# Kernel tuning notes

Hardware: AMD Instinct MI355X
Metric: run time of the kernel (lower is better)

The kernel has to match this reference:

```python
import jax, jax.numpy as jnp
import numpy as np

D_MODEL, D_FF, N_EXPERTS, TOP_K = 1024, 4096, 8, 2
LN_EPS = 1e-5


def setup_inputs() -> dict:
    key = jax.random.key(0)
    ks = jax.random.split(key, 9)
    s = 0.02
    return {
        "x": jax.random.normal(ks[0], (4, 2048, D_MODEL), dtype=jnp.float32),
        "Wg": jax.random.normal(ks[1], (D_MODEL, N_EXPERTS), dtype=jnp.float32) * s,
        "bg": jnp.zeros((N_EXPERTS,), dtype=jnp.float32),
        "W1": jax.random.normal(ks[2], (N_EXPERTS, D_MODEL, D_FF), dtype=jnp.float32) * s,
        "b1": jnp.zeros((N_EXPERTS, D_FF), dtype=jnp.float32),
        "W2": jax.random.normal(ks[3], (N_EXPERTS, D_FF, D_MODEL), dtype=jnp.float32) * s,
        "b2": jnp.zeros((N_EXPERTS, D_MODEL), dtype=jnp.float32),
        "gamma": jnp.ones((D_MODEL,), dtype=jnp.float32),
        "beta": jnp.zeros((D_MODEL,), dtype=jnp.float32),
    }


def _moe(x, Wg, bg, W1, b1, W2, b2, gamma, beta):
    B, S, D = x.shape
    xf = x.reshape(B * S, D)                       # (T, D)
    logits = xf @ Wg + bg                          # (T, E)
    probs = jax.nn.softmax(logits, axis=-1)
    topk_scores, topk_idx = jax.lax.top_k(probs, TOP_K)   # (T, K)
    # combine weights per expert: w[t, e] = sum_k score[t,k] * [idx[t,k]==e]
    onehot = jax.nn.one_hot(topk_idx, N_EXPERTS, dtype=probs.dtype)  # (T, K, E)
    w = jnp.einsum("tk,tke->te", topk_scores, onehot)                # (T, E)
    # load-balancing aux loss (switch-style): E * sum_e f_e * P_e
    f = jnp.mean(onehot, axis=(0, 1)) * 1.0        # fraction of routed slots per expert
    P = jnp.mean(probs, axis=0)
    aux_loss = jnp.float32(N_EXPERTS) * jnp.sum(f * P)
    # dense-equivalent expert compute; zero weight for unrouted tokens matches
    # the masked gather/scatter math of the original.
    out = jnp.zeros_like(xf)
    for e in range(N_EXPERTS):
        h = jax.nn.relu(xf @ W1[e] + b1[e])        # (T, D_FF)
        y = h @ W2[e] + b2[e]                      # (T, D)
        out = out + w[:, e:e + 1] * y
    out = out.reshape(B, S, D)
    # residual + post-layernorm (dropout disabled, eval mode)
    z = x + out
    mu = jnp.mean(z, axis=-1, keepdims=True)
    var = jnp.mean(jnp.square(z - mu), axis=-1, keepdims=True)
    z = (z - mu) * jax.lax.rsqrt(var + LN_EPS) * gamma + beta
    return z, aux_loss


def reference(x, Wg, bg, W1, b1, W2, b2, gamma, beta):
    return _moe(x, Wg, bg, W1, b1, W2, b2, gamma, beta)
```

## Files before the change

### kernel.cpp

```cpp
#include <hip/hip_runtime.h>

#define T_TOK 8192
#define DM    1024
#define DFF   4096
#define NE    8
#define CAP   2560
#define SLOTS (NE * CAP)
#define MTILES 20

typedef __attribute__((ext_vector_type(4))) float f32x4;
typedef __attribute__((ext_vector_type(8))) short bf16x8;
typedef __attribute__((ext_vector_type(4))) unsigned short u16x4;

__device__ __forceinline__ unsigned short f2bf(float f) {
  unsigned int u = __float_as_uint(f);
  u = (u + 0x7FFFu + ((u >> 16) & 1u)) >> 16;
  return (unsigned short)u;
}
__device__ __forceinline__ float bf2f(unsigned short u) {
  return __uint_as_float(((unsigned)u) << 16);
}

__device__ __forceinline__ void gld_lds16(const void* g, void* l) {
  __builtin_amdgcn_global_load_lds(
      (const __attribute__((address_space(1))) void*)g,
      (__attribute__((address_space(3))) void*)l, 16, 0, 0);
}

__device__ __forceinline__ bf16x8 ldsr(unsigned addr) {
  bf16x8 r;
  asm volatile("ds_read_b128 %0, %1" : "=v"(r) : "v"(addr));
  return r;
}

__global__ __launch_bounds__(256) void transpose_convert2(
    const float* __restrict__ W1, unsigned short* __restrict__ W1t,
    const float* __restrict__ W2, unsigned short* __restrict__ W2t)
{
  __shared__ float tile[64][65];
  int z = blockIdx.z;
  const float* W; unsigned short* Wt; int R, C, c0, r0;
  if (z < 8) {
    W = W1 + (size_t)z * DM * DFF; Wt = W1t + (size_t)z * DM * DFF;
    R = DM; C = DFF;
    c0 = blockIdx.x * 64; r0 = blockIdx.y * 64;
  } else {
    W = W2 + (size_t)(z - 8) * DM * DFF; Wt = W2t + (size_t)(z - 8) * DM * DFF;
    R = DFF; C = DM;
    c0 = (blockIdx.x & 15) * 64; r0 = (blockIdx.y * 4 + (blockIdx.x >> 4)) * 64;
  }
  int tid = threadIdx.x;
  int lr = tid >> 4, lc = (tid & 15) * 4;
#pragma unroll
  for (int i = 0; i < 4; ++i) {
    float4 v = *(const float4*)(W + (size_t)(r0 + i * 16 + lr) * C + c0 + lc);
    tile[i * 16 + lr][lc] = v.x; tile[i * 16 + lr][lc + 1] = v.y;
    tile[i * 16 + lr][lc + 2] = v.z; tile[i * 16 + lr][lc + 3] = v.w;
  }
  __syncthreads();
#pragma unroll
  for (int i = 0; i < 4; ++i) {
    int o = i * 256 + tid;
    int rq = o & 15, cw = o >> 4;
    u16x4 u;
    u.x = f2bf(tile[rq * 4 + 0][cw]); u.y = f2bf(tile[rq * 4 + 1][cw]);
    u.z = f2bf(tile[rq * 4 + 2][cw]); u.w = f2bf(tile[rq * 4 + 3][cw]);
    __builtin_nontemporal_store(u, (u16x4*)(Wt + (size_t)(c0 + cw) * R + r0 + rq * 4));
  }
}

__global__ __launch_bounds__(256) void router_kernel(
    const float* __restrict__ x, const float* __restrict__ Wg, const float* __restrict__ bg,
    int* __restrict__ slotOf, float* __restrict__ slot_w,
    int* __restrict__ pos, float* __restrict__ P_sh,
    unsigned short* __restrict__ Abuf)
{
  __shared__ float wgT[NE * DM];
  for (int i = threadIdx.x; i < NE * DM; i += 256) {
    int d = i >> 3, e = i & 7;
    wgT[e * DM + d] = Wg[i];
  }
  __syncthreads();
  int w = threadIdx.x >> 6, lane = threadIdx.x & 63;
  int sh = blockIdx.x & 63;
  for (int it = 0; it < 4; ++it) {
    int t = (blockIdx.x * 4 + w) * 4 + it;
    float4 xv[4];
    float p[NE];
#pragma unroll
    for (int e = 0; e < NE; ++e) p[e] = 0.f;
#pragma unroll
    for (int ps = 0; ps < 4; ++ps) {
      int d0 = ps * 256 + lane * 4;
      xv[ps] = *(const float4*)(x + (size_t)t * DM + d0);
#pragma unroll
      for (int e = 0; e < NE; ++e) {
        float4 wv = *(const float4*)(wgT + e * DM + d0);
        p[e] += xv[ps].x * wv.x + xv[ps].y * wv.y + xv[ps].z * wv.z + xv[ps].w * wv.w;
      }
    }
#pragma unroll
    for (int e = 0; e < NE; ++e) {
#pragma unroll
      for (int o = 1; o < 64; o <<= 1) p[e] += __shfl_xor(p[e], o);
      p[e] += bg[e];
    }
    float mx = p[0];
#pragma unroll
    for (int e = 1; e < NE; ++e) mx = fmaxf(mx, p[e]);
    float se = 0.f;
#pragma unroll
    for (int e = 0; e < NE; ++e) { p[e] = expf(p[e] - mx); se += p[e]; }
    float inv = 1.f / se;
#pragma unroll
    for (int e = 0; e < NE; ++e) p[e] *= inv;
    int e0 = 0; float v0 = p[0];
#pragma unroll
    for (int e = 1; e < NE; ++e) if (p[e] > v0) { v0 = p[e]; e0 = e; }
    int e1 = -1; float v1 = -1.f;
#pragma unroll
    for (int e = 0; e < NE; ++e) if (e != e0 && p[e] > v1) { v1 = p[e]; e1 = e; }
    int p0 = 0, p1 = 0;
    if (lane == 0) {
      p0 = atomicAdd(&pos[e0], 1);
      p1 = atomicAdd(&pos[e1], 1);
    }
    p0 = __shfl(p0, 0); p1 = __shfl(p1, 0);
    int s0 = e0 * CAP + (p0 < CAP ? p0 : CAP - 1);
    int s1 = e1 * CAP + (p1 < CAP ? p1 : CAP - 1);
    if (lane == 0) {
      slotOf[2 * t] = s0; slotOf[2 * t + 1] = s1;
      slot_w[s0] = v0; slot_w[s1] = v1;
#pragma unroll
      for (int e = 0; e < NE; ++e) atomicAdd(&P_sh[sh * 8 + e], p[e]);
    }
    unsigned short* d0p = Abuf + (size_t)s0 * DM;
    unsigned short* d1p = Abuf + (size_t)s1 * DM;
#pragma unroll
    for (int ps = 0; ps < 4; ++ps) {
      int d = ps * 256 + lane * 4;
      ushort4 u;
      u.x = f2bf(xv[ps].x); u.y = f2bf(xv[ps].y);
      u.z = f2bf(xv[ps].z); u.w = f2bf(xv[ps].w);
      *(ushort4*)(d0p + d) = u;
      *(ushort4*)(d1p + d) = u;
    }
  }
}

template<int KDIM, int EPI>
__global__ __launch_bounds__(256, 3) void moe_gemm(
    const unsigned short* __restrict__ A, const unsigned short* __restrict__ Bt,
    const float* __restrict__ bias, unsigned short* __restrict__ Out,
    const int* __restrict__ pos, const float* __restrict__ slot_w, int N)
{
  constexpr int KT = (EPI == 0 ? KDIM : KDIM / 2) / 32;
  int e, koff, sp;
  if (EPI == 0) { e = blockIdx.z; koff = 0; sp = 0; }
  else { e = blockIdx.z >> 1; sp = blockIdx.z & 1; koff = sp * (KDIM / 2); }

  int cnt = pos[e];
  if (cnt > CAP) cnt = CAP;

  int nx = N >> 7;
  int b = blockIdx.x + blockIdx.y * nx;
  int cpx = nx * MTILES / 8;
  int wg = (b & 7) * cpx + (b >> 3);
  int ntile = wg / MTILES, mt = wg % MTILES;
  if (mt * 128 >= cnt) return;
  int m0 = e * CAP + mt * 128, n0 = ntile * 128;

  __shared__ __align__(16) char lds[49152];

  const int tid = threadIdx.x, lane = tid & 63, w = tid >> 6;
  const int wr = w >> 1, wc = w & 1;

  const int ssl = 8 * ((tid & 3) ^ ((tid >> 3) & 3));
  const unsigned short* Asrc = A + (size_t)(m0 + (tid >> 2)) * KDIM + koff + ssl;
  const unsigned short* Bsrc = Bt + (size_t)e * N * KDIM + (size_t)(n0 + (tid >> 2)) * KDIM + koff + ssl;

  unsigned lbase = (unsigned)(size_t)(__attribute__((address_space(3))) char*)lds;
  const unsigned swz = 16u * (unsigned)((lane >> 4) ^ ((lane >> 1) & 3));
  const unsigned aoff = (unsigned)((wr * 64 + (lane & 15)) * 64) + swz;
  const unsigned boff = 8192u + (unsigned)((wc * 64 + (lane & 15)) * 64) + swz;

  f32x4 acc[4][4] = {};
  bf16x8 Aq[4], Bq[4];

#define STAGE(KT_, BUFO_)                                                    \
  { int k0_ = (KT_) * 32;                                                    \
    char* lb_ = lds + (BUFO_);                                               \
    gld_lds16(Asrc + k0_,                      lb_ + tid * 16);              \
    gld_lds16(Asrc + (size_t)64 * KDIM + k0_,  lb_ + 4096 + tid * 16);       \
    gld_lds16(Bsrc + k0_,                      lb_ + 8192 + tid * 16);       \
    gld_lds16(Bsrc + (size_t)64 * KDIM + k0_,  lb_ + 12288 + tid * 16); }

  STAGE(0, 0)
  STAGE(1, 16384)
  asm volatile("s_waitcnt vmcnt(4)" ::: "memory");
  __builtin_amdgcn_s_barrier();

  unsigned cur = 0;
#pragma unroll 1
  for (int kt = 0; kt < KT; ++kt) {
    unsigned bo = lbase + cur;
    if (kt + 2 < KT) {
      unsigned stg = cur + 32768u; if (stg >= 49152u) stg -= 49152u;
      STAGE(kt + 2, stg)
    }
#pragma unroll
    for (int mi = 0; mi < 4; ++mi) Aq[mi] = ldsr(bo + aoff + mi * 1024u);
#pragma unroll
    for (int ni = 0; ni < 4; ++ni) Bq[ni] = ldsr(bo + boff + ni * 1024u);
    asm volatile("s_waitcnt lgkmcnt(0)" ::: "memory");
    __builtin_amdgcn_sched_barrier(0);
    __builtin_amdgcn_s_setprio(1);
#pragma unroll
    for (int mi = 0; mi < 4; ++mi)
#pragma unroll
      for (int ni = 0; ni < 4; ++ni)
        acc[mi][ni] = __builtin_amdgcn_mfma_f32_16x16x32_bf16(
            Aq[mi], Bq[ni], acc[mi][ni], 0, 0, 0);
    __builtin_amdgcn_s_setprio(0);
    if (kt + 2 < KT)      asm volatile("s_waitcnt vmcnt(4)" ::: "memory");
    else if (kt + 1 < KT) asm volatile("s_waitcnt vmcnt(0)" ::: "memory");
    __builtin_amdgcn_s_barrier();
    cur += 16384u; if (cur == 49152u) cur = 0;
  }
#undef STAGE

  int cn = lane & 15;
  int r4 = (lane >> 4) * 4;
  if (EPI == 0) {
#pragma unroll
    for (int ni = 0; ni < 4; ++ni) {
      int col = n0 + wc * 64 + ni * 16 + cn;
      float bv = bias[e * N + col];
#pragma unroll
      for (int mi = 0; mi < 4; ++mi) {
        int row = m0 + wr * 64 + mi * 16 + r4;
#pragma unroll
        for (int j = 0; j < 4; ++j) {
          float v = acc[mi][ni][j] + bv;
          __builtin_nontemporal_store(f2bf(v > 0.f ? v : 0.f),
                                      Out + (size_t)(row + j) * N + col);
        }
      }
    }
  } else {
    unsigned short* Yw = Out + (size_t)sp * SLOTS * DM;
    float bv[4];
#pragma unroll
    for (int ni = 0; ni < 4; ++ni)
      bv[ni] = (sp == 0) ? bias[e * N + n0 + wc * 64 + ni * 16 + cn] : 0.f;
#pragma unroll
    for (int mi = 0; mi < 4; ++mi) {
      int rbase = m0 + wr * 64 + mi * 16 + r4;
#pragma unroll
      for (int j = 0; j < 4; ++j) {
        int slot = rbase + j;
        float wgt = slot_w[slot];
#pragma unroll
        for (int ni = 0; ni < 4; ++ni) {
          int col = n0 + wc * 64 + ni * 16 + cn;
          __builtin_nontemporal_store(f2bf(wgt * (acc[mi][ni][j] + bv[ni])),
                                      Yw + (size_t)slot * DM + col);
        }
      }
    }
  }
}

__global__ __launch_bounds__(256) void ln_kernel(
    const float* __restrict__ x, const unsigned short* __restrict__ Ybuf,
    const int* __restrict__ slotOf,
    const float* __restrict__ gamma, const float* __restrict__ beta,
    float* __restrict__ out)
{
  int t = blockIdx.x;
  int s0 = slotOf[2 * t], s1 = slotOf[2 * t + 1];
  const unsigned short* y00 = Ybuf + (size_t)s0 * DM;
  const unsigned short* y01 = Ybuf + (size_t)SLOTS * DM + (size_t)s0 * DM;
  const unsigned short* y10 = Ybuf + (size_t)s1 * DM;
  const unsigned short* y11 = Ybuf + (size_t)SLOTS * DM + (size_t)s1 * DM;
  int c = threadIdx.x * 4;
  float4 xv = *(const float4*)(x + (size_t)t * DM + c);
  ushort4 a0 = *(const ushort4*)(y00 + c);
  ushort4 a1 = *(const ushort4*)(y01 + c);
  ushort4 a2 = *(const ushort4*)(y10 + c);
  ushort4 a3 = *(const ushort4*)(y11 + c);
  float z[4];
  z[0] = xv.x + bf2f(a0.x) + bf2f(a1.x) + bf2f(a2.x) + bf2f(a3.x);
  z[1] = xv.y + bf2f(a0.y) + bf2f(a1.y) + bf2f(a2.y) + bf2f(a3.y);
  z[2] = xv.z + bf2f(a0.z) + bf2f(a1.z) + bf2f(a2.z) + bf2f(a3.z);
  z[3] = xv.w + bf2f(a0.w) + bf2f(a1.w) + bf2f(a2.w) + bf2f(a3.w);
  float s = z[0] + z[1] + z[2] + z[3];
  float s2 = z[0]*z[0] + z[1]*z[1] + z[2]*z[2] + z[3]*z[3];
#pragma unroll
  for (int o = 1; o < 64; o <<= 1) { s += __shfl_xor(s, o); s2 += __shfl_xor(s2, o); }
  __shared__ float ls[8];
  int w = threadIdx.x >> 6, lane = threadIdx.x & 63;
  if (lane == 0) { ls[w] = s; ls[4 + w] = s2; }
  __syncthreads();
  s = ls[0] + ls[1] + ls[2] + ls[3];
  s2 = ls[4] + ls[5] + ls[6] + ls[7];
  float mu = s * (1.f / DM);
  float var = s2 * (1.f / DM) - mu * mu;
  float rstd = rsqrtf(var + 1e-5f);
  float4 gv = *(const float4*)(gamma + c);
  float4 bv = *(const float4*)(beta + c);
  float4 ov;
  ov.x = (z[0] - mu) * rstd * gv.x + bv.x;
  ov.y = (z[1] - mu) * rstd * gv.y + bv.y;
  ov.z = (z[2] - mu) * rstd * gv.z + bv.z;
  ov.w = (z[3] - mu) * rstd * gv.w + bv.w;
  *(float4*)(out + (size_t)t * DM + c) = ov;
}

__global__ void aux_kernel(const float* __restrict__ P_sh,
                           const int* __restrict__ pos, float* __restrict__ out_aux)
{
  if (threadIdx.x == 0) {
    float aux = 0.f;
    for (int e = 0; e < NE; ++e) {
      float P = 0.f;
      for (int i = 0; i < 64; ++i) P += P_sh[i * 8 + e];
      P *= (1.f / T_TOK);
      float f = pos[e] * (1.f / (T_TOK * 2));
      aux += f * P;
    }
    out_aux[0] = (float)NE * aux;
  }
}

extern "C" void kernel_launch(void* const* d_in, const int* in_sizes, int n_in,
                              void* d_out, int out_size, void* d_ws, size_t ws_size,
                              hipStream_t stream)
{
  (void)in_sizes; (void)n_in; (void)out_size; (void)ws_size;
  const float* x     = (const float*)d_in[0];
  const float* Wg    = (const float*)d_in[1];
  const float* bg    = (const float*)d_in[2];
  const float* W1    = (const float*)d_in[3];
  const float* b1    = (const float*)d_in[4];
  const float* W2    = (const float*)d_in[5];
  const float* b2    = (const float*)d_in[6];
  const float* gamma = (const float*)d_in[7];
  const float* beta  = (const float*)d_in[8];
  float* out = (float*)d_out;

  char* ws = (char*)d_ws;
  size_t off = 0;
  auto alloc = [&](size_t bytes) -> void* {
    void* p = ws + off;
    off += (bytes + 255) & ~(size_t)255;
    return p;
  };
  int*   pos      = (int*)alloc(8 * 4);
  float* P_sh     = (float*)alloc(64 * 8 * 4);
  size_t meta_end = off;
  int*   slotOf   = (int*)alloc(16384 * 4);
  float* slot_w   = (float*)alloc((size_t)SLOTS * 4);
  unsigned short* Hbuf = (unsigned short*)alloc((size_t)SLOTS * DFF * 2);
  unsigned short* W2t  = (unsigned short*)alloc((size_t)NE * DM * DFF * 2);
  unsigned short* Abuf = (unsigned short*)alloc((size_t)SLOTS * DM * 2);
  unsigned short* W1t  = (unsigned short*)alloc((size_t)2 * SLOTS * DM * 2);
  unsigned short* Ybuf = W1t;

  (void)hipMemsetAsync(d_ws, 0, meta_end, stream);

  transpose_convert2<<<dim3(64, 16, 16), 256, 0, stream>>>(W1, W1t, W2, W2t);
  router_kernel<<<512, 256, 0, stream>>>(x, Wg, bg, slotOf, slot_w, pos, P_sh, Abuf);
  moe_gemm<DM, 0><<<dim3(32, MTILES, 8), 256, 0, stream>>>(
      Abuf, W1t, b1, Hbuf, pos, slot_w, DFF);
  moe_gemm<DFF, 1><<<dim3(8, MTILES, 16), 256, 0, stream>>>(
      Hbuf, W2t, b2, Ybuf, pos, slot_w, DM);
  ln_kernel<<<T_TOK, 256, 0, stream>>>(x, Ybuf, slotOf, gamma, beta, out);
  aux_kernel<<<1, 64, 0, stream>>>(P_sh, pos, out + (size_t)T_TOK * DM);
}
```

Measured before the change: 727.4 us.

## Fuse prep kernels, gather GEMM1 rows by token index, shrink pipeline for occupancy

Merges the weight transpose/convert and router into one launch, and has the router write a single bf16 copy of x plus a slot-to-token map instead of scattering duplicated rows. The first expert GEMM gathers its A rows via that map. Both GEMMs switch from a three-stage to a two-stage LDS pipeline with smaller shared memory and a higher occupancy hint. This trades prefetch depth for more resident blocks and removes a scatter write, at the risk of exposed load latency.

Result: slower. 1.240 ms (+70.5%).

```diff
diff --git a/kernel.cpp b/kernel.cpp
--- a/kernel.cpp
+++ b/kernel.cpp
@@ -33,58 +33,59 @@
   return r;
 }
 
-__global__ __launch_bounds__(256) void transpose_convert2(
+__global__ __launch_bounds__(256) void prep_kernel(
     const float* __restrict__ W1, unsigned short* __restrict__ W1t,
-    const float* __restrict__ W2, unsigned short* __restrict__ W2t)
-{
-  __shared__ float tile[64][65];
-  int z = blockIdx.z;
-  const float* W; unsigned short* Wt; int R, C, c0, r0;
-  if (z < 8) {
-    W = W1 + (size_t)z * DM * DFF; Wt = W1t + (size_t)z * DM * DFF;
-    R = DM; C = DFF;
-    c0 = blockIdx.x * 64; r0 = blockIdx.y * 64;
-  } else {
-    W = W2 + (size_t)(z - 8) * DM * DFF; Wt = W2t + (size_t)(z - 8) * DM * DFF;
-    R = DFF; C = DM;
-    c0 = (blockIdx.x & 15) * 64; r0 = (blockIdx.y * 4 + (blockIdx.x >> 4)) * 64;
-  }
+    const float* __restrict__ W2, unsigned short* __restrict__ W2t,
+    const float* __restrict__ x, const float* __restrict__ Wg, const float* __restrict__ bg,
+    unsigned short* __restrict__ xbf, int* __restrict__ slot_tok,
+    int* __restrict__ slotOf, float* __restrict__ slot_w,
+    int* __restrict__ pos, float* __restrict__ P_sh)
+{
+  __shared__ __align__(16) char smem[32768];
   int tid = threadIdx.x;
-  int lr = tid >> 4, lc = (tid & 15) * 4;
-#pragma unroll
-  for (int i = 0; i < 4; ++i) {
-    float4 v = *(const float4*)(W + (size_t)(r0 + i * 16 + lr) * C + c0 + lc);
-    tile[i * 16 + lr][lc] = v.x; tile[i * 16 + lr][lc + 1] = v.y;
-    tile[i * 16 + lr][lc + 2] = v.z; tile[i * 16 + lr][lc + 3] = v.w;
-  }
-  __syncthreads();
-#pragma unroll
-  for (int i = 0; i < 4; ++i) {
-    int o = i * 256 + tid;
-    int rq = o & 15, cw = o >> 4;
-    u16x4 u;
-    u.x = f2bf(tile[rq * 4 + 0][cw]); u.y = f2bf(tile[rq * 4 + 1][cw]);
-    u.z = f2bf(tile[rq * 4 + 2][cw]); u.w = f2bf(tile[rq * 4 + 3][cw]);
-    __builtin_nontemporal_store(u, (u16x4*)(Wt + (size_t)(c0 + cw) * R + r0 + rq * 4));
-  }
-}
-
-__global__ __launch_bounds__(256) void router_kernel(
-    const float* __restrict__ x, const float* __restrict__ Wg, const float* __restrict__ bg,
-    int* __restrict__ slotOf, float* __restrict__ slot_w,
-    int* __restrict__ pos, float* __restrict__ P_sh,
-    unsigned short* __restrict__ Abuf)
-{
-  __shared__ float wgT[NE * DM];
-  for (int i = threadIdx.x; i < NE * DM; i += 256) {
+  if (blockIdx.x < 16384) {
+    float (*tile)[65] = (float(*)[65])smem;
+    int bx = blockIdx.x & 63, by = (blockIdx.x >> 6) & 15, z = blockIdx.x >> 10;
+    const float* W; unsigned short* Wt; int R, C, c0, r0;
+    if (z < 8) {
+      W = W1 + (size_t)z * DM * DFF; Wt = W1t + (size_t)z * DM * DFF;
+      R = DM; C = DFF;
+      c0 = bx * 64; r0 = by * 64;
+    } else {
+      W = W2 + (size_t)(z - 8) * DM * DFF; Wt = W2t + (size_t)(z - 8) * DM * DFF;
+      R = DFF; C = DM;
+      c0 = (bx & 15) * 64; r0 = (by * 4 + (bx >> 4)) * 64;
+    }
+    int lr = tid >> 4, lc = (tid & 15) * 4;
+#pragma unroll
+    for (int i = 0; i < 4; ++i) {
+      float4 v = *(const float4*)(W + (size_t)(r0 + i * 16 + lr) * C + c0 + lc);
+      tile[i * 16 + lr][lc] = v.x; tile[i * 16 + lr][lc + 1] = v.y;
+      tile[i * 16 + lr][lc + 2] = v.z; tile[i * 16 + lr][lc + 3] = v.w;
+    }
+    __syncthreads();
+#pragma unroll
+    for (int i = 0; i < 4; ++i) {
+      int o = i * 256 + tid;
+      int rq = o & 15, cw = o >> 4;
+      u16x4 u;
+      u.x = f2bf(tile[rq * 4 + 0][cw]); u.y = f2bf(tile[rq * 4 + 1][cw]);
+      u.z = f2bf(tile[rq * 4 + 2][cw]); u.w = f2bf(tile[rq * 4 + 3][cw]);
+      __builtin_nontemporal_store(u, (u16x4*)(Wt + (size_t)(c0 + cw) * R + r0 + rq * 4));
+    }
+    return;
+  }
+  float* wgT = (float*)smem;
+  int rid = blockIdx.x - 16384;
+  for (int i = tid; i < NE * DM; i += 256) {
     int d = i >> 3, e = i & 7;
     wgT[e * DM + d] = Wg[i];
   }
   __syncthreads();
-  int w = threadIdx.x >> 6, lane = threadIdx.x & 63;
-  int sh = blockIdx.x & 63;
+  int w = tid >> 6, lane = tid & 63;
+  int sh = rid & 63;
   for (int it = 0; it < 4; ++it) {
-    int t = (blockIdx.x * 4 + w) * 4 + it;
+    int t = (rid * 4 + w) * 4 + it;
     float4 xv[4];
     float p[NE];
 #pragma unroll
@@ -130,29 +131,29 @@
     int s1 = e1 * CAP + (p1 < CAP ? p1 : CAP - 1);
     if (lane == 0) {
       slotOf[2 * t] = s0; slotOf[2 * t + 1] = s1;
-      slot_w[s0] = v0; slot_w[s1] = v1;
+      slot_tok[s0] = t;  slot_tok[s1] = t;
+      slot_w[s0] = v0;   slot_w[s1] = v1;
 #pragma unroll
       for (int e = 0; e < NE; ++e) atomicAdd(&P_sh[sh * 8 + e], p[e]);
     }
-    unsigned short* d0p = Abuf + (size_t)s0 * DM;
-    unsigned short* d1p = Abuf + (size_t)s1 * DM;
+    unsigned short* xr = xbf + (size_t)t * DM;
 #pragma unroll
     for (int ps = 0; ps < 4; ++ps) {
       int d = ps * 256 + lane * 4;
       ushort4 u;
       u.x = f2bf(xv[ps].x); u.y = f2bf(xv[ps].y);
       u.z = f2bf(xv[ps].z); u.w = f2bf(xv[ps].w);
-      *(ushort4*)(d0p + d) = u;
-      *(ushort4*)(d1p + d) = u;
+      *(ushort4*)(xr + d) = u;
     }
   }
 }
 
 template<int KDIM, int EPI>
-__global__ __launch_bounds__(256, 3) void moe_gemm(
+__global__ __launch_bounds__(256, 5) void moe_gemm(
     const unsigned short* __restrict__ A, const unsigned short* __restrict__ Bt,
     const float* __restrict__ bias, unsigned short* __restrict__ Out,
-    const int* __restrict__ pos, const float* __restrict__ slot_w, int N)
+    const int* __restrict__ pos, const float* __restrict__ slot_w,
+    const int* __restrict__ slot_tok, int N)
 {
   constexpr int KT = (EPI == 0 ? KDIM : KDIM / 2) / 32;
   int e, koff, sp;
@@ -170,14 +171,20 @@
   if (mt * 128 >= cnt) return;
   int m0 = e * CAP + mt * 128, n0 = ntile * 128;
 
-  __shared__ __align__(16) char lds[49152];
+  __shared__ __align__(16) char lds[32768];
 
   const int tid = threadIdx.x, lane = tid & 63, w = tid >> 6;
   const int wr = w >> 1, wc = w & 1;
 
   const int ssl = 8 * ((tid & 3) ^ ((tid >> 3) & 3));
-  const unsigned short* Asrc = A + (size_t)(m0 + (tid >> 2)) * KDIM + koff + ssl;
-  const unsigned short* Bsrc = Bt + (size_t)e * N * KDIM + (size_t)(n0 + (tid >> 2)) * KDIM + koff + ssl;
+  int r0 = m0 + (tid >> 2);
+  size_t ar0, ar1;
+  if (EPI == 0) { ar0 = (size_t)slot_tok[r0]; ar1 = (size_t)slot_tok[r0 + 64]; }
+  else          { ar0 = (size_t)r0;           ar1 = (size_t)(r0 + 64); }
+  const unsigned short* A0 = A + ar0 * KDIM + koff + ssl;
+  const unsigned short* A1 = A + ar1 * KDIM + koff + ssl;
+  const unsigned short* B0 = Bt + (size_t)e * N * KDIM + (size_t)(n0 + (tid >> 2)) * KDIM + koff + ssl;
+  const unsigned short* B1 = B0 + (size_t)64 * KDIM;
 
   unsigned lbase = (unsigned)(size_t)(__attribute__((address_space(3))) char*)lds;
   const unsigned swz = 16u * (unsigned)((lane >> 4) ^ ((lane >> 1) & 3));
@@ -190,24 +197,19 @@
 #define STAGE(KT_, BUFO_)                                                    \
   { int k0_ = (KT_) * 32;                                                    \
     char* lb_ = lds + (BUFO_);                                               \
-    gld_lds16(Asrc + k0_,                      lb_ + tid * 16);              \
-    gld_lds16(Asrc + (size_t)64 * KDIM + k0_,  lb_ + 4096 + tid * 16);       \
-    gld_lds16(Bsrc + k0_,                      lb_ + 8192 + tid * 16);       \
-    gld_lds16(Bsrc + (size_t)64 * KDIM + k0_,  lb_ + 12288 + tid * 16); }
+    gld_lds16(A0 + k0_, lb_ + tid * 16);                                     \
+    gld_lds16(A1 + k0_, lb_ + 4096 + tid * 16);                              \
+    gld_lds16(B0 + k0_, lb_ + 8192 + tid * 16);                              \
+    gld_lds16(B1 + k0_, lb_ + 12288 + tid * 16); }
 
   STAGE(0, 0)
-  STAGE(1, 16384)
-  asm volatile("s_waitcnt vmcnt(4)" ::: "memory");
+  asm volatile("s_waitcnt vmcnt(0)" ::: "memory");
   __builtin_amdgcn_s_barrier();
 
-  unsigned cur = 0;
 #pragma unroll 1
   for (int kt = 0; kt < KT; ++kt) {
-    unsigned bo = lbase + cur;
-    if (kt + 2 < KT) {
-      unsigned stg = cur + 32768u; if (stg >= 49152u) stg -= 49152u;
-      STAGE(kt + 2, stg)
-    }
+    unsigned bo = lbase + (unsigned)((kt & 1) * 16384);
+    if (kt + 1 < KT) STAGE(kt + 1, ((kt + 1) & 1) * 16384)
 #pragma unroll
     for (int mi = 0; mi < 4; ++mi) Aq[mi] = ldsr(bo + aoff + mi * 1024u);
 #pragma unroll
@@ -222,10 +224,8 @@
         acc[mi][ni] = __builtin_amdgcn_mfma_f32_16x16x32_bf16(
             Aq[mi], Bq[ni], acc[mi][ni], 0, 0, 0);
     __builtin_amdgcn_s_setprio(0);
-    if (kt + 2 < KT)      asm volatile("s_waitcnt vmcnt(4)" ::: "memory");
-    else if (kt + 1 < KT) asm volatile("s_waitcnt vmcnt(0)" ::: "memory");
+    if (kt + 1 < KT) asm volatile("s_waitcnt vmcnt(0)" ::: "memory");
     __builtin_amdgcn_s_barrier();
-    cur += 16384u; if (cur == 49152u) cur = 0;
   }
 #undef STAGE
 
@@ -358,23 +358,24 @@
   };
   int*   pos      = (int*)alloc(8 * 4);
   float* P_sh     = (float*)alloc(64 * 8 * 4);
+  int*   slot_tok = (int*)alloc((size_t)SLOTS * 4);
   size_t meta_end = off;
   int*   slotOf   = (int*)alloc(16384 * 4);
   float* slot_w   = (float*)alloc((size_t)SLOTS * 4);
+  unsigned short* xbf  = (unsigned short*)alloc((size_t)T_TOK * DM * 2);
   unsigned short* Hbuf = (unsigned short*)alloc((size_t)SLOTS * DFF * 2);
   unsigned short* W2t  = (unsigned short*)alloc((size_t)NE * DM * DFF * 2);
-  unsigned short* Abuf = (unsigned short*)alloc((size_t)SLOTS * DM * 2);
   unsigned short* W1t  = (unsigned short*)alloc((size_t)2 * SLOTS * DM * 2);
   unsigned short* Ybuf = W1t;
 
   (void)hipMemsetAsync(d_ws, 0, meta_end, stream);
 
-  transpose_convert2<<<dim3(64, 16, 16), 256, 0, stream>>>(W1, W1t, W2, W2t);
-  router_kernel<<<512, 256, 0, stream>>>(x, Wg, bg, slotOf, slot_w, pos, P_sh, Abuf);
+  prep_kernel<<<16896, 256, 0, stream>>>(W1, W1t, W2, W2t, x, Wg, bg,
+                                         xbf, slot_tok, slotOf, slot_w, pos, P_sh);
   moe_gemm<DM, 0><<<dim3(32, MTILES, 8), 256, 0, stream>>>(
-      Abuf, W1t, b1, Hbuf, pos, slot_w, DFF);
+      xbf, W1t, b1, Hbuf, pos, slot_w, slot_tok, DFF);
   moe_gemm<DFF, 1><<<dim3(8, MTILES, 16), 256, 0, stream>>>(
-      Hbuf, W2t, b2, Ybuf, pos, slot_w, DM);
+      Hbuf, W2t, b2, Ybuf, pos, slot_w, slot_tok, DM);
   ln_kernel<<<T_TOK, 256, 0, stream>>>(x, Ybuf, slotOf, gamma, beta, out);
   aux_kernel<<<1, 64, 0, stream>>>(P_sh, pos, out + (size_t)T_TOK * DM);
 }
```
